# Kernel tuning notes

Measured on AMD Instinct MI355X. Metric: run time of the kernel, lower is better.

Reference implementation:

```python
import jax, jax.numpy as jnp
import numpy as np

BLOCK = 128
FP8_MAX = 448.0  # max finite value of float8_e4m3fn


def _quant_weight(w, key_unused=None):
    """Per-128x128-block FP8 quantization of weight [N, K].
    Returns (w_q_as_f32, scale[N//128, K//128])."""
    N, K = w.shape
    nb, kb = N // BLOCK, K // BLOCK
    wb = w.reshape(nb, BLOCK, kb, BLOCK)
    amax = jnp.max(jnp.abs(wb), axis=(1, 3))  # [nb, kb]
    scale = jnp.maximum(amax, 1e-12) / FP8_MAX
    w_q = (wb / scale[:, None, :, None]).astype(jnp.float8_e4m3fn).astype(jnp.float32)
    return w_q.reshape(N, K), scale.astype(jnp.float32)


def setup_inputs() -> dict:
    key = jax.random.key(0)
    k1, k2 = jax.random.split(key)
    B, S, K, N = 2, 2048, 7168, 4096
    x = jax.random.normal(k1, (B, S, K), dtype=jnp.float32)
    w_master = jax.random.normal(k2, (N, K), dtype=jnp.float32) * 0.02
    weight, weight_scale = _quant_weight(w_master)
    return {"x": x, "weight": weight, "weight_scale": weight_scale}


def act_quant(x):
    """Per-128-element block quant along last dim. Returns (x_q_f32, scale[..., K//128])."""
    *lead, K = x.shape
    kb = K // BLOCK
    xb = x.reshape(*lead, kb, BLOCK)
    amax = jnp.max(jnp.abs(xb), axis=-1)  # [..., kb]
    scale = jnp.maximum(amax, 1e-12) / FP8_MAX
    x_q = (xb / scale[..., None]).astype(jnp.float8_e4m3fn).astype(jnp.float32)
    return x_q.reshape(*lead, K), scale


def reference(x, weight, weight_scale):
    # 1) blockwise FP8 activation quant
    x_q, a_scale = act_quant(x)  # x_q: [B,S,K], a_scale: [B,S,K//128]
    # 2) dequant-equivalent GEMM: y[m,n] = sum_k x_q[m,k]*a_s[m,blk(k)] * w_q[n,k]*w_s[blk(n),blk(k)]
    x_deq = x_q * jnp.repeat(a_scale, BLOCK, axis=-1)  # [B,S,K]
    w_deq = weight * jnp.repeat(jnp.repeat(weight_scale, BLOCK, axis=0), BLOCK, axis=1)  # [N,K]
    y = jnp.einsum('bsk,nk->bsn', x_deq, w_deq)
    return y
```

## Files before the change

kernel.cpp:

```cpp
#include <hip/hip_runtime.h>

#define K_DIM 7168
#define N_DIM 4096
#define KBLKS 56
#define FP8MAX 448.0f

typedef float f32x4 __attribute__((ext_vector_type(4)));

#define GLOBAL_AS __attribute__((address_space(1)))
#define LDS_AS __attribute__((address_space(3)))

__device__ __forceinline__ void gload_lds16(const void* g, void* l) {
  __builtin_amdgcn_global_load_lds((GLOBAL_AS void*)g, (LDS_AS void*)l, 16, 0, 0);
}

__device__ __forceinline__ int pack_fp8x4(float a, float b, float c, float d) {
  int v = __builtin_amdgcn_cvt_pk_fp8_f32(a, b, 0, false);
  v = __builtin_amdgcn_cvt_pk_fp8_f32(c, d, v, true);
  return v;
}

__global__ void quant_x_kernel(const float* __restrict__ x,
                               unsigned char* __restrict__ xq,
                               float* __restrict__ asT, int M) {
  int gid = (int)((blockIdx.x * blockDim.x + threadIdx.x) >> 5);
  int lane = threadIdx.x & 31;
  if (gid >= M * KBLKS) return;
  int m = gid / KBLKS;
  int kb = gid - m * KBLKS;
  size_t off = (size_t)m * K_DIM + kb * 128 + lane * 4;
  float4 v = *(const float4*)(x + off);
  float amax = fmaxf(fmaxf(fabsf(v.x), fabsf(v.y)), fmaxf(fabsf(v.z), fabsf(v.w)));
#pragma unroll
  for (int d = 16; d; d >>= 1) amax = fmaxf(amax, __shfl_xor(amax, d));
  float scale = fmaxf(amax, 1e-12f) / FP8MAX;
  int pk = pack_fp8x4(v.x / scale, v.y / scale, v.z / scale, v.w / scale);
  *(int*)(xq + off) = pk;
  if (lane == 0) asT[(size_t)kb * M + m] = scale;
}

__global__ void quant_w_kernel(const float* __restrict__ w,
                               unsigned char* __restrict__ wq, long n4) {
  long i = (long)blockIdx.x * blockDim.x + threadIdx.x;
  if (i >= n4) return;
  float4 v = *(const float4*)(w + i * 4);
  ((int*)wq)[i] = pack_fp8x4(v.x, v.y, v.z, v.w);
}

__global__ __launch_bounds__(256, 2)
void gemm_fp8_blk(const unsigned char* __restrict__ xq,
                  const unsigned char* __restrict__ wq,
                  const float* __restrict__ asT,
                  const float* __restrict__ wscale,
                  float* __restrict__ out, int M) {
  __shared__ unsigned char ldsA[128 * 128];
  __shared__ unsigned char ldsB[128 * 128];
  __shared__ float ldsAS[128];

  const int bid = blockIdx.x;
  const int per = gridDim.x >> 3;
  const int swz = (bid & 7) * per + (bid >> 3);
  const int bn = swz & ((N_DIM / 128) - 1);
  const int bm = swz / (N_DIM / 128);
  const int m0 = bm * 128, n0 = bn * 128;

  const int tid = threadIdx.x;
  const int wv = tid >> 6, lane = tid & 63;
  const int wm = (wv >> 1) * 64, wn = (wv & 1) * 64;

  f32x4 acc[4][4] = {};

  auto stage = [&](int kb) {
#pragma unroll
    for (int i = 0; i < 4; ++i) {
      int o = i * 4096 + wv * 1024 + lane * 16;
      int row = o >> 7;
      int col = (o & 127) ^ ((row & 7) << 4);
      gload_lds16(xq + (size_t)(m0 + row) * K_DIM + (size_t)kb * 128 + col,
                  ldsA + i * 4096 + wv * 1024);
    }
#pragma unroll
    for (int i = 0; i < 4; ++i) {
      int o = i * 4096 + wv * 1024 + lane * 16;
      int row = o >> 7;
      int col = (o & 127) ^ ((row & 7) << 4);
      gload_lds16(wq + (size_t)(n0 + row) * K_DIM + (size_t)kb * 128 + col,
                  ldsB + i * 4096 + wv * 1024);
    }
    if (tid < 128) ldsAS[tid] = asT[(size_t)kb * M + m0 + tid];
  };

  stage(0);

  const int wsrow = bn * KBLKS;
  const int rsel = lane & 15;
  const int ksel = (lane >> 4) << 3;
  const int jrow = (lane >> 4) << 2;

  for (int kb = 0; kb < KBLKS; ++kb) {
    __syncthreads();

    f32x4 as4[4];
#pragma unroll
    for (int mi = 0; mi < 4; ++mi)
      as4[mi] = *(const f32x4*)&ldsAS[wm + mi * 16 + jrow];

    long af[4][4], bf[4][4];
#pragma unroll
    for (int kk = 0; kk < 4; ++kk) {
#pragma unroll
      for (int i = 0; i < 4; ++i) {
        int rowa = wm + i * 16 + rsel;
        int cola = (kk * 32 + ksel) ^ ((rowa & 7) << 4);
        af[kk][i] = *(const long*)(ldsA + rowa * 128 + cola);
        int rowb = wn + i * 16 + rsel;
        int colb = (kk * 32 + ksel) ^ ((rowb & 7) << 4);
        bf[kk][i] = *(const long*)(ldsB + rowb * 128 + colb);
      }
    }
    __syncthreads();

    if (kb + 1 < KBLKS) stage(kb + 1);

    float wsc = wscale[wsrow + kb];
#pragma unroll
    for (int mi = 0; mi < 4; ++mi) {
      f32x4 comb = as4[mi] * wsc;
#pragma unroll
      for (int ni = 0; ni < 4; ++ni) {
        f32x4 t = {0.f, 0.f, 0.f, 0.f};
#pragma unroll
        for (int kk = 0; kk < 4; ++kk)
          t = __builtin_amdgcn_mfma_f32_16x16x32_fp8_fp8(af[kk][mi], bf[kk][ni], t, 0, 0, 0);
        acc[mi][ni] += t * comb;
      }
    }
  }

#pragma unroll
  for (int mi = 0; mi < 4; ++mi) {
#pragma unroll
    for (int j = 0; j < 4; ++j) {
      int rowm = m0 + wm + mi * 16 + jrow + j;
      float* op = out + (size_t)rowm * N_DIM + n0 + wn + rsel;
#pragma unroll
      for (int ni = 0; ni < 4; ++ni) op[ni * 16] = acc[mi][ni][j];
    }
  }
}

extern "C" void kernel_launch(void* const* d_in, const int* in_sizes, int n_in,
                              void* d_out, int out_size, void* d_ws, size_t ws_size,
                              hipStream_t stream) {
  const float* x    = (const float*)d_in[0];
  const float* wgt  = (const float*)d_in[1];
  const float* wsc  = (const float*)d_in[2];
  float* out = (float*)d_out;

  const int K = K_DIM, N = N_DIM;
  const int M = in_sizes[0] / K;

  unsigned char* xq = (unsigned char*)d_ws;
  unsigned char* wq = xq + (size_t)M * K;
  float* asT = (float*)(wq + (size_t)N * K);

  int groups = M * (K / 128);
  quant_x_kernel<<<(groups * 32 + 255) / 256, 256, 0, stream>>>(x, xq, asT, M);
  quant_w_kernel<<<((long)N * K / 4 + 255) / 256, 256, 0, stream>>>(wgt, wq, (long)N * K / 4);

  dim3 grid((M / 128) * (N / 128));
  gemm_fp8_blk<<<grid, 256, 0, stream>>>(xq, wq, asT, wsc, out, M);
}
```

Measured before the change: 496.6 us.

## Use 256x256 double-buffered FP8 GEMM tiles and fuse quant kernels

The GEMM moves from 128x128 tiles with 4 waves to 256x256 tiles with 8 waves, and LDS is now double-buffered. Next-tile global-to-LDS loads are interleaved with the MFMA phases, using barriers and s_setprio, and the activation scale is also loaded straight into LDS. The two quantization kernels are merged into one launch. The aim is higher arithmetic intensity per loaded byte and hiding load latency behind compute, at the cost of 128KB of LDS per block, more registers and only 256 blocks, which may leave CUs underused.

```diff
diff --git a/kernel.cpp b/kernel.cpp
--- a/kernel.cpp
+++ b/kernel.cpp
@@ -4,6 +4,8 @@
 #define N_DIM 4096
 #define KBLKS 56
 #define FP8MAX 448.0f
+#define BM 256
+#define BN 256
 
 typedef float f32x4 __attribute__((ext_vector_type(4)));
 
@@ -20,11 +22,18 @@
   return v;
 }
 
-__global__ void quant_x_kernel(const float* __restrict__ x,
-                               unsigned char* __restrict__ xq,
-                               float* __restrict__ asT, int M) {
-  int gid = (int)((blockIdx.x * blockDim.x + threadIdx.x) >> 5);
-  int lane = threadIdx.x & 31;
+__global__ void quant_fused(const float* __restrict__ x, const float* __restrict__ w,
+                            unsigned char* __restrict__ xq, unsigned char* __restrict__ wq,
+                            float* __restrict__ asT, int M, long nw4) {
+  long gidx = (long)blockIdx.x * blockDim.x + threadIdx.x;
+  if (gidx < nw4) {
+    float4 v = *(const float4*)(w + gidx * 4);
+    ((int*)wq)[gidx] = pack_fp8x4(v.x, v.y, v.z, v.w);
+    return;
+  }
+  long t = gidx - nw4;
+  int gid = (int)(t >> 5);
+  int lane = (int)t & 31;
   if (gid >= M * KBLKS) return;
   int m = gid / KBLKS;
   int kb = gid - m * KBLKS;
@@ -34,115 +43,136 @@
 #pragma unroll
   for (int d = 16; d; d >>= 1) amax = fmaxf(amax, __shfl_xor(amax, d));
   float scale = fmaxf(amax, 1e-12f) / FP8MAX;
-  int pk = pack_fp8x4(v.x / scale, v.y / scale, v.z / scale, v.w / scale);
-  *(int*)(xq + off) = pk;
+  *(int*)(xq + off) = pack_fp8x4(v.x / scale, v.y / scale, v.z / scale, v.w / scale);
   if (lane == 0) asT[(size_t)kb * M + m] = scale;
 }
 
-__global__ void quant_w_kernel(const float* __restrict__ w,
-                               unsigned char* __restrict__ wq, long n4) {
-  long i = (long)blockIdx.x * blockDim.x + threadIdx.x;
-  if (i >= n4) return;
-  float4 v = *(const float4*)(w + i * 4);
-  ((int*)wq)[i] = pack_fp8x4(v.x, v.y, v.z, v.w);
-}
-
-__global__ __launch_bounds__(256, 2)
+__global__ __launch_bounds__(512, 2)
 void gemm_fp8_blk(const unsigned char* __restrict__ xq,
                   const unsigned char* __restrict__ wq,
                   const float* __restrict__ asT,
                   const float* __restrict__ wscale,
                   float* __restrict__ out, int M) {
-  __shared__ unsigned char ldsA[128 * 128];
-  __shared__ unsigned char ldsB[128 * 128];
-  __shared__ float ldsAS[128];
+  __shared__ unsigned char ldsA[2][32768];
+  __shared__ unsigned char ldsB[2][32768];
+  __shared__ float ldsAS[2][256];
 
   const int bid = blockIdx.x;
-  const int per = gridDim.x >> 3;
+  const int nbn = N_DIM / BN;
+  const int per = (M / BM) * nbn >> 3;
   const int swz = (bid & 7) * per + (bid >> 3);
-  const int bn = swz & ((N_DIM / 128) - 1);
-  const int bm = swz / (N_DIM / 128);
-  const int m0 = bm * 128, n0 = bn * 128;
+  const int m0 = (swz / nbn) * BM, n0 = (swz % nbn) * BN;
 
   const int tid = threadIdx.x;
   const int wv = tid >> 6, lane = tid & 63;
-  const int wm = (wv >> 1) * 64, wn = (wv & 1) * 64;
-
-  f32x4 acc[4][4] = {};
-
-  auto stage = [&](int kb) {
-#pragma unroll
-    for (int i = 0; i < 4; ++i) {
-      int o = i * 4096 + wv * 1024 + lane * 16;
-      int row = o >> 7;
-      int col = (o & 127) ^ ((row & 7) << 4);
-      gload_lds16(xq + (size_t)(m0 + row) * K_DIM + (size_t)kb * 128 + col,
-                  ldsA + i * 4096 + wv * 1024);
-    }
-#pragma unroll
-    for (int i = 0; i < 4; ++i) {
-      int o = i * 4096 + wv * 1024 + lane * 16;
-      int row = o >> 7;
-      int col = (o & 127) ^ ((row & 7) << 4);
-      gload_lds16(wq + (size_t)(n0 + row) * K_DIM + (size_t)kb * 128 + col,
-                  ldsB + i * 4096 + wv * 1024);
-    }
-    if (tid < 128) ldsAS[tid] = asT[(size_t)kb * M + m0 + tid];
+  const int wm = (wv >> 2) * 128;
+  const int wn = (wv & 3) * 64;
+  const int rsel = lane & 15;
+  const int ks = lane >> 4;
+  const int j0 = ks >> 1, h8 = (ks & 1) * 8;
+  const int jrow = ks * 4;
+
+  int swk[4];
+#pragma unroll
+  for (int kk = 0; kk < 4; ++kk)
+    swk[kk] = (((kk * 2 + j0) ^ (rsel & 7)) * 16) + h8;
+
+  int srow[4], scol[4];
+#pragma unroll
+  for (int it = 0; it < 4; ++it) {
+    int o = it * 8192 + wv * 1024 + lane * 16;
+    int r = o >> 7, sl = (o >> 4) & 7;
+    srow[it] = r;
+    scol[it] = (sl ^ (r & 7)) * 16;
+  }
+
+  f32x4 acc[8][4] = {};
+
+  auto stageA = [&](int t1, int b, int it) {
+    gload_lds16(xq + (size_t)(m0 + srow[it]) * K_DIM + (size_t)t1 * 128 + scol[it],
+                &ldsA[b][it * 8192 + wv * 1024]);
   };
-
-  stage(0);
-
-  const int wsrow = bn * KBLKS;
-  const int rsel = lane & 15;
-  const int ksel = (lane >> 4) << 3;
-  const int jrow = (lane >> 4) << 2;
-
-  for (int kb = 0; kb < KBLKS; ++kb) {
-    __syncthreads();
-
-    f32x4 as4[4];
-#pragma unroll
-    for (int mi = 0; mi < 4; ++mi)
-      as4[mi] = *(const f32x4*)&ldsAS[wm + mi * 16 + jrow];
-
-    long af[4][4], bf[4][4];
-#pragma unroll
-    for (int kk = 0; kk < 4; ++kk) {
-#pragma unroll
-      for (int i = 0; i < 4; ++i) {
-        int rowa = wm + i * 16 + rsel;
-        int cola = (kk * 32 + ksel) ^ ((rowa & 7) << 4);
-        af[kk][i] = *(const long*)(ldsA + rowa * 128 + cola);
-        int rowb = wn + i * 16 + rsel;
-        int colb = (kk * 32 + ksel) ^ ((rowb & 7) << 4);
-        bf[kk][i] = *(const long*)(ldsB + rowb * 128 + colb);
+  auto stageB = [&](int t1, int b, int it) {
+    gload_lds16(wq + (size_t)(n0 + srow[it]) * K_DIM + (size_t)t1 * 128 + scol[it],
+                &ldsB[b][it * 8192 + wv * 1024]);
+  };
+  auto stageS = [&](int t1, int b) {
+    if (wv == 0) gload_lds16(asT + (size_t)t1 * M + m0 + lane * 4, &ldsAS[b][0]);
+  };
+
+#pragma unroll
+  for (int it = 0; it < 4; ++it) { stageA(0, 0, it); stageB(0, 0, it); }
+  stageS(0, 0);
+  asm volatile("s_waitcnt vmcnt(0)" ::: "memory");
+  __builtin_amdgcn_s_barrier();
+
+  for (int t = 0; t < KBLKS; ++t) {
+    const int cur = t & 1;
+    const unsigned char* pA0 = &ldsA[cur][(wm + rsel) * 128];
+    const unsigned char* pB0 = &ldsB[cur][(wn + rsel) * 128];
+    const float wsv = wscale[(size_t)((n0 + wn) >> 7) * KBLKS + t];
+    const bool pf = (t + 1 < KBLKS);
+
+#pragma unroll
+    for (int mh = 0; mh < 2; ++mh) {
+#pragma unroll
+      for (int nh = 0; nh < 2; ++nh) {
+        f32x4 tmp[4][2];
+#pragma unroll
+        for (int kh = 0; kh < 2; ++kh) {
+          const int p = mh * 4 + nh * 2 + kh;
+          long a[4][2], b[2][2];
+#pragma unroll
+          for (int mi = 0; mi < 4; ++mi)
+#pragma unroll
+            for (int q = 0; q < 2; ++q)
+              a[mi][q] = *(const long*)(pA0 + mh * 8192 + mi * 2048 + swk[kh * 2 + q]);
+#pragma unroll
+          for (int ni = 0; ni < 2; ++ni)
+#pragma unroll
+            for (int q = 0; q < 2; ++q)
+              b[ni][q] = *(const long*)(pB0 + nh * 4096 + ni * 2048 + swk[kh * 2 + q]);
+
+          if (pf) {
+            if (p == 0) { stageA(t + 1, cur ^ 1, 0); stageA(t + 1, cur ^ 1, 1); stageS(t + 1, cur ^ 1); }
+            if (p == 1) { stageA(t + 1, cur ^ 1, 2); stageA(t + 1, cur ^ 1, 3); }
+            if (p == 2) { stageB(t + 1, cur ^ 1, 0); stageB(t + 1, cur ^ 1, 1); }
+            if (p == 3) { stageB(t + 1, cur ^ 1, 2); stageB(t + 1, cur ^ 1, 3); }
+          }
+          __builtin_amdgcn_s_barrier();
+          __builtin_amdgcn_s_setprio(1);
+#pragma unroll
+          for (int mi = 0; mi < 4; ++mi)
+#pragma unroll
+            for (int ni = 0; ni < 2; ++ni) {
+              f32x4 t4 = (kh == 0) ? (f32x4){0.f, 0.f, 0.f, 0.f} : tmp[mi][ni];
+              t4 = __builtin_amdgcn_mfma_f32_16x16x32_fp8_fp8(a[mi][0], b[ni][0], t4, 0, 0, 0);
+              t4 = __builtin_amdgcn_mfma_f32_16x16x32_fp8_fp8(a[mi][1], b[ni][1], t4, 0, 0, 0);
+              tmp[mi][ni] = t4;
+            }
+          __builtin_amdgcn_s_setprio(0);
+          __builtin_amdgcn_s_barrier();
+        }
+        const float* pAS = &ldsAS[cur][wm + mh * 64 + jrow];
+#pragma unroll
+        for (int mi = 0; mi < 4; ++mi) {
+          f32x4 as4 = *(const f32x4*)(pAS + mi * 16);
+          f32x4 comb = as4 * wsv;
+#pragma unroll
+          for (int ni = 0; ni < 2; ++ni)
+            acc[mh * 4 + mi][nh * 2 + ni] += tmp[mi][ni] * comb;
+        }
       }
     }
-    __syncthreads();
-
-    if (kb + 1 < KBLKS) stage(kb + 1);
-
-    float wsc = wscale[wsrow + kb];
-#pragma unroll
-    for (int mi = 0; mi < 4; ++mi) {
-      f32x4 comb = as4[mi] * wsc;
-#pragma unroll
-      for (int ni = 0; ni < 4; ++ni) {
-        f32x4 t = {0.f, 0.f, 0.f, 0.f};
-#pragma unroll
-        for (int kk = 0; kk < 4; ++kk)
-          t = __builtin_amdgcn_mfma_f32_16x16x32_fp8_fp8(af[kk][mi], bf[kk][ni], t, 0, 0, 0);
-        acc[mi][ni] += t * comb;
-      }
-    }
-  }
-
-#pragma unroll
-  for (int mi = 0; mi < 4; ++mi) {
+    asm volatile("s_waitcnt vmcnt(0)" ::: "memory");
+    __builtin_amdgcn_s_barrier();
+  }
+
+#pragma unroll
+  for (int mi = 0; mi < 8; ++mi) {
 #pragma unroll
     for (int j = 0; j < 4; ++j) {
-      int rowm = m0 + wm + mi * 16 + jrow + j;
-      float* op = out + (size_t)rowm * N_DIM + n0 + wn + rsel;
+      float* op = out + (size_t)(m0 + wm + mi * 16 + jrow + j) * N_DIM + n0 + wn + rsel;
 #pragma unroll
       for (int ni = 0; ni < 4; ++ni) op[ni * 16] = acc[mi][ni][j];
     }
@@ -152,9 +182,9 @@
 extern "C" void kernel_launch(void* const* d_in, const int* in_sizes, int n_in,
                               void* d_out, int out_size, void* d_ws, size_t ws_size,
                               hipStream_t stream) {
-  const float* x    = (const float*)d_in[0];
-  const float* wgt  = (const float*)d_in[1];
-  const float* wsc  = (const float*)d_in[2];
+  const float* x   = (const float*)d_in[0];
+  const float* wgt = (const float*)d_in[1];
+  const float* wsc = (const float*)d_in[2];
   float* out = (float*)d_out;
 
   const int K = K_DIM, N = N_DIM;
@@ -164,10 +194,11 @@
   unsigned char* wq = xq + (size_t)M * K;
   float* asT = (float*)(wq + (size_t)N * K);
 
-  int groups = M * (K / 128);
-  quant_x_kernel<<<(groups * 32 + 255) / 256, 256, 0, stream>>>(x, xq, asT, M);
-  quant_w_kernel<<<((long)N * K / 4 + 255) / 256, 256, 0, stream>>>(wgt, wq, (long)N * K / 4);
-
-  dim3 grid((M / 128) * (N / 128));
-  gemm_fp8_blk<<<grid, 256, 0, stream>>>(xq, wq, asT, wsc, out, M);
-}
+  long nw4 = (long)N * K / 4;
+  long nx  = (long)M * KBLKS * 32;
+  long tot = nw4 + nx;
+  quant_fused<<<(int)((tot + 255) / 256), 256, 0, stream>>>(x, wgt, xq, wq, asT, M, nw4);
+
+  dim3 grid((M / BM) * (N / BN));
+  gemm_fp8_blk<<<grid, 512, 0, stream>>>(xq, wq, asT, wsc, out, M);
+}
```

New measurement: 543.8 us. 1.09x slower.
